# Optimization experiments

Measured on AMD Instinct MI355X. Metric: run time of the kernel, lower is better.

Reference implementation:

```python
import jax, jax.numpy as jnp
import numpy as np

E, TOPK, HID, FFN = 8, 2, 1024, 2048  # experts, top_k, hidden K, intermediate N
B, S = 2, 1024


def setup_inputs() -> dict:
    key = jax.random.key(0)
    ks = jax.random.split(key, 7)
    return {
        "x": jax.random.normal(ks[0], (B, S, HID), jnp.float32),
        "router_weight": jax.random.normal(ks[1], (E, HID), jnp.float32) * 0.02,
        "router_bias": jax.random.normal(ks[2], (E,), jnp.float32) * 0.02,
        "w1": jax.random.normal(ks[3], (E, 2 * FFN, HID), jnp.float32) * 0.02,  # [E,2N,K] gate|up
        "w1_bias": jax.random.normal(ks[4], (E, 2 * FFN), jnp.float32) * 0.02,
        "w2": jax.random.normal(ks[5], (E, HID, FFN), jnp.float32) * 0.02,      # [E,K,N]
        "w2_bias": jax.random.normal(ks[6], (E, HID), jnp.float32) * 0.02,
        "top_k": TOPK,
    }


def reference(x, router_weight, router_bias, w1, w1_bias, w2, w2_bias, top_k):
    Bb, Ss, K = x.shape
    xf = x.reshape(-1, K)                                   # [M,K]
    M = xf.shape[0]
    Ne = w1.shape[0]
    # --- route_tokens: softmax over experts, then top-k (megablocks style) ---
    logits = xf @ router_weight.T + router_bias             # [M,E]
    probs = jax.nn.softmax(logits, axis=-1)
    topk_w, topk_ids = jax.lax.top_k(probs, top_k)          # [M,topk]
    # combine weights: scatter top-k probs into dense [M,E]
    comb = jnp.zeros((M, Ne), xf.dtype).at[jnp.arange(M)[:, None], topk_ids].add(topk_w)
    # --- fused experts (dense combine formulation, same math as grouped GEMM) ---
    gu = jnp.einsum('mk,enk->men', xf, w1) + w1_bias[None]  # [M,E,2N]
    Nf = gu.shape[-1] // 2
    gate, up = gu[..., :Nf], gu[..., Nf:]
    h = jax.nn.silu(gate) * up                              # silu_and_mul (SwiGLU)
    down = jnp.einsum('men,ekn->mek', h, w2) + w2_bias[None]  # [M,E,K]
    out = jnp.einsum('mek,me->mk', down, comb)              # weighted combine
    return out.reshape(Bb, Ss, K), topk_w
```

## Files before the change

kernel.cpp:

```cpp
#include <hip/hip_runtime.h>
#include <hip/hip_bf16.h>
#include <math.h>

#define E_    8
#define HID_  1024
#define FFN_  2048
#define M_    2048
#define NP2_  (E_*M_)

typedef __attribute__((ext_vector_type(8))) short bf16x8;
typedef __attribute__((ext_vector_type(8))) short short8v;
typedef __attribute__((ext_vector_type(4))) float f32x4;
typedef __attribute__((ext_vector_type(4))) int   i32x4;

typedef const __attribute__((address_space(1))) void GVOID;
typedef __attribute__((address_space(3))) void LVOID;

#define VMCNT4 asm volatile("s_waitcnt vmcnt(4)" ::: "memory")
#define VMCNT0 asm volatile("s_waitcnt vmcnt(0)" ::: "memory")

__device__ __forceinline__ short f2bf(float f) {
    union { __hip_bfloat16 b; short s; } u;
    u.b = __float2bfloat16(f);
    return u.s;
}

__device__ __forceinline__ bf16x8 pk8(f32x4 lo, f32x4 hi) {
    unsigned u0, u1, u2, u3;
    asm("v_cvt_pk_bf16_f32 %0, %1, %2" : "=v"(u0) : "v"(lo.x), "v"(lo.y));
    asm("v_cvt_pk_bf16_f32 %0, %1, %2" : "=v"(u1) : "v"(lo.z), "v"(lo.w));
    asm("v_cvt_pk_bf16_f32 %0, %1, %2" : "=v"(u2) : "v"(hi.x), "v"(hi.y));
    asm("v_cvt_pk_bf16_f32 %0, %1, %2" : "=v"(u3) : "v"(hi.z), "v"(hi.w));
    union { i32x4 i; bf16x8 b; } r;
    r.i = (i32x4){(int)u0, (int)u1, (int)u2, (int)u3};
    return r.b;
}

__global__ __launch_bounds__(64) void router_kernel(
    const float* __restrict__ x, const float* __restrict__ rw,
    const float* __restrict__ rb, int* __restrict__ fill,
    int* __restrict__ gtok, float* __restrict__ gwt, int* __restrict__ pos,
    float* __restrict__ topk_out, __hip_bfloat16* __restrict__ xb)
{
    const int m    = blockIdx.x;
    const int lane = threadIdx.x;
    const float4* xm4 = (const float4*)(x + (size_t)m * HID_);

    float4 xv[4];
#pragma unroll
    for (int j = 0; j < 4; ++j) xv[j] = xm4[j*64 + lane];

    short4* xbr = (short4*)(xb + (size_t)m * HID_);
#pragma unroll
    for (int j = 0; j < 4; ++j) {
        short4 o;
        o.x = f2bf(xv[j].x); o.y = f2bf(xv[j].y);
        o.z = f2bf(xv[j].z); o.w = f2bf(xv[j].w);
        xbr[j*64 + lane] = o;
    }

    float lg[E_];
#pragma unroll
    for (int e = 0; e < E_; ++e) {
        const float4* we4 = (const float4*)(rw + e * HID_);
        float s = 0.f;
#pragma unroll
        for (int j = 0; j < 4; ++j) {
            float4 w = we4[j*64 + lane];
            s = fmaf(xv[j].x, w.x, s);
            s = fmaf(xv[j].y, w.y, s);
            s = fmaf(xv[j].z, w.z, s);
            s = fmaf(xv[j].w, w.w, s);
        }
        lg[e] = s;
    }
#pragma unroll
    for (int off = 32; off; off >>= 1)
#pragma unroll
        for (int e = 0; e < E_; ++e) lg[e] += __shfl_xor(lg[e], off);

    if (lane == 0) {
        float l2[E_], p[E_];
        float mx = -1e30f;
#pragma unroll
        for (int e = 0; e < E_; ++e) { l2[e] = lg[e] + rb[e]; mx = fmaxf(mx, l2[e]); }
        float sum = 0.f;
#pragma unroll
        for (int e = 0; e < E_; ++e) { p[e] = expf(l2[e] - mx); sum += p[e]; }
        float inv = 1.f / sum;
#pragma unroll
        for (int e = 0; e < E_; ++e) p[e] *= inv;

        int   i1 = -1, i2 = -1;
        float v1 = -1e30f, v2 = -1e30f;
#pragma unroll
        for (int e = 0; e < E_; ++e) {
            float pe = p[e];
            if (pe > v1)      { v2 = v1; i2 = i1; v1 = pe; i1 = e; }
            else if (pe > v2) { v2 = pe; i2 = e; }
        }
        topk_out[2*m]   = v1;
        topk_out[2*m+1] = v2;
        int p1s = atomicAdd(&fill[i1], 1);
        int s1  = i1*M_ + p1s;
        gtok[s1] = m; gwt[s1] = v1; pos[2*m]   = s1;
        int p2s = atomicAdd(&fill[i2], 1);
        int s2  = i2*M_ + p2s;
        gtok[s2] = m; gwt[s2] = v2; pos[2*m+1] = s2;
    }
}

__global__ __launch_bounds__(256, 3) void gemm1_kernel(
    const __hip_bfloat16* __restrict__ xb, const float* __restrict__ w1,
    const float* __restrict__ w1b, const int* __restrict__ gtok,
    const int* __restrict__ fill, __hip_bfloat16* __restrict__ h,
    const float* __restrict__ w2, __hip_bfloat16* __restrict__ w2bf)
{
    const int e  = blockIdx.z;
    const int ce = fill[e];
    const int t0 = blockIdx.y * 128;

    if (blockIdx.y >= 8) {
        int cid = blockIdx.x + 32*(blockIdx.y - 8) + 256*e;
        const float4* src = (const float4*)w2;
        short8v* dst = (short8v*)w2bf;
        size_t c0 = (size_t)cid * 1024;
#pragma unroll
        for (int u = 0; u < 4; ++u) {
            size_t c = c0 + u*256 + threadIdx.x;
            float4 a = src[2*c];
            float4 b = src[2*c + 1];
            short8v o;
            o[0] = f2bf(a.x); o[1] = f2bf(a.y); o[2] = f2bf(a.z); o[3] = f2bf(a.w);
            o[4] = f2bf(b.x); o[5] = f2bf(b.y); o[6] = f2bf(b.z); o[7] = f2bf(b.w);
            dst[c] = o;
        }
    }

    if (t0 >= ce) return;
    const int n0   = blockIdx.x * 64;
    const int base = e * M_;
    const float* w1e = w1 + (size_t)e * (2*FFN_) * HID_;

    __shared__ __align__(16) __hip_bfloat16 As[2][128*32];
    __shared__ __align__(16) float          Bsf[2][128*32];

    const int tid  = threadIdx.x;
    const int lane = tid & 63;
    const int wid  = tid >> 6;
    const int wm   = wid >> 1;
    const int wn   = wid & 1;
    const int cf   = lane >> 4;

    const __hip_bfloat16* asrc[2];
#pragma unroll
    for (int q = 0; q < 2; ++q) {
        int slot = q*256 + tid;
        int r = slot >> 2, p = slot & 3;
        int c = p ^ ((r >> 1) & 3);
        int rr  = min(t0 + r, ce - 1);
        asrc[q] = xb + (size_t)gtok[base + rr] * HID_ + c*8;
    }
    const float* bsrc[4];
#pragma unroll
    for (int q = 0; q < 4; ++q) {
        int slot = q*256 + tid;
        int r = slot >> 3, p = slot & 7;
        int c = p ^ (r & 7);
        int q2 = r >> 5, s = r & 31;
        int grow = (q2 & 1) ? (FFN_ + n0 + (q2>>1)*32 + s)
                            : (       n0 + (q2>>1)*32 + s);
        bsrc[q] = w1e + (size_t)grow * HID_ + c*4;
    }

    auto STAGE = [&](int b, int k0) {
#pragma unroll
        for (int q = 0; q < 2; ++q)
            __builtin_amdgcn_global_load_lds((GVOID*)(asrc[q] + k0),
                (LVOID*)(&As[b][(q*256 + wid*64)*8]), 16, 0, 0);
#pragma unroll
        for (int q = 0; q < 4; ++q)
            __builtin_amdgcn_global_load_lds((GVOID*)(bsrc[q] + k0),
                (LVOID*)(&Bsf[b][(q*256 + wid*64)*4]), 16, 0, 0);
    };

    f32x4 acc[4][4];
#pragma unroll
    for (int m = 0; m < 4; ++m)
#pragma unroll
        for (int n = 0; n < 4; ++n) acc[m][n] = (f32x4){0.f,0.f,0.f,0.f};

    auto COMPUTE = [&](int cb) {
        bf16x8 af[4], bfr[4];
#pragma unroll
        for (int m = 0; m < 4; ++m) {
            int r = wm*64 + m*16 + (lane & 15);
            int sw = cf ^ ((r >> 1) & 3);
            af[m] = *(bf16x8*)&As[cb][r*32 + sw*8];
        }
#pragma unroll
        for (int n = 0; n < 4; ++n) {
            int r = wn*64 + n*16 + (lane & 15);
            int p0 = (2*cf)     ^ (r & 7);
            int p1 = (2*cf + 1) ^ (r & 7);
            f32x4 lo = *(f32x4*)&Bsf[cb][r*32 + p0*4];
            f32x4 hi = *(f32x4*)&Bsf[cb][r*32 + p1*4];
            bfr[n] = pk8(lo, hi);
        }
        __builtin_amdgcn_s_setprio(1);
#pragma unroll
        for (int m = 0; m < 4; ++m)
#pragma unroll
            for (int n = 0; n < 4; ++n)
                acc[m][n] = __builtin_amdgcn_mfma_f32_16x16x32_bf16(
                    af[m], bfr[n], acc[m][n], 0, 0, 0);
        __builtin_amdgcn_s_setprio(0);
    };

    const int NT = HID_/32;
    STAGE(0, 0);
    __syncthreads();
    for (int t = 0; t < NT; ++t) {
        int cur = t & 1, nxt = cur ^ 1;
        if (t + 1 < NT) STAGE(nxt, (t+1)*32);
        COMPUTE(cur);
        __syncthreads();
    }

    const float* w1be = w1b + e*2*FFN_;
#pragma unroll
    for (int n = 0; n < 2; ++n) {
        int col = n0 + wn*32 + n*16 + (lane & 15);
        float bg = w1be[col];
        float bu = w1be[FFN_ + col];
#pragma unroll
        for (int m = 0; m < 4; ++m) {
            int rb2 = t0 + wm*64 + m*16 + (lane >> 4)*4;
#pragma unroll
            for (int i = 0; i < 4; ++i) {
                int t = rb2 + i;
                if (t < ce) {
                    float g = acc[m][n][i]   + bg;
                    float u = acc[m][n+2][i] + bu;
                    float hv = (g / (1.f + __expf(-g))) * u;
                    h[(size_t)(base + t)*FFN_ + col] = __float2bfloat16(hv);
                }
            }
        }
    }
}

__global__ __launch_bounds__(256, 3) void gemm2_kernel(
    const __hip_bfloat16* __restrict__ h, const __hip_bfloat16* __restrict__ w2bf,
    const float* __restrict__ w2b, const float* __restrict__ gwt,
    const int* __restrict__ fill, float* __restrict__ dpair)
{
    const int e  = blockIdx.z & 7;
    const int ks = blockIdx.z >> 3;
    const int ce = fill[e];
    const int t0 = blockIdx.y * 128;
    if (t0 >= ce) return;
    const int n0    = blockIdx.x * 128;
    const int base  = e * M_;
    const int kbase = ks * (FFN_/2);
    const __hip_bfloat16* w2e = w2bf + (size_t)e * HID_ * FFN_;

    __shared__ __align__(16) __hip_bfloat16 As[3][128*32];
    __shared__ __align__(16) __hip_bfloat16 Bs[3][128*32];

    const int tid  = threadIdx.x;
    const int lane = tid & 63;
    const int wid  = tid >> 6;
    const int wm   = wid >> 1;
    const int wn   = wid & 1;

    const __hip_bfloat16 *asrc[2], *bsrc[2];
#pragma unroll
    for (int q = 0; q < 2; ++q) {
        int slot = q*256 + tid;
        int r = slot >> 2, p = slot & 3;
        int c = p ^ ((r >> 1) & 3);
        int rr = min(t0 + r, ce - 1);
        asrc[q] = h   + (size_t)(base + rr) * FFN_ + kbase + c*8;
        bsrc[q] = w2e + (size_t)(n0 + r)    * FFN_ + kbase + c*8;
    }

    auto STAGE = [&](int b, int k0) {
#pragma unroll
        for (int q = 0; q < 2; ++q)
            __builtin_amdgcn_global_load_lds((GVOID*)(asrc[q] + k0),
                (LVOID*)(&As[b][(q*256 + wid*64)*8]), 16, 0, 0);
#pragma unroll
        for (int q = 0; q < 2; ++q)
            __builtin_amdgcn_global_load_lds((GVOID*)(bsrc[q] + k0),
                (LVOID*)(&Bs[b][(q*256 + wid*64)*8]), 16, 0, 0);
    };

    f32x4 acc[4][4];
#pragma unroll
    for (int m = 0; m < 4; ++m)
#pragma unroll
        for (int n = 0; n < 4; ++n) acc[m][n] = (f32x4){0.f,0.f,0.f,0.f};

    const int cf = lane >> 4;
    auto COMPUTE = [&](int cb) {
        bf16x8 af[4], bfr[4];
#pragma unroll
        for (int m = 0; m < 4; ++m) {
            int r = wm*64 + m*16 + (lane & 15);
            int sw = cf ^ ((r >> 1) & 3);
            af[m] = *(bf16x8*)&As[cb][r*32 + sw*8];
        }
#pragma unroll
        for (int n = 0; n < 4; ++n) {
            int r = wn*64 + n*16 + (lane & 15);
            int sw = cf ^ ((r >> 1) & 3);
            bfr[n] = *(bf16x8*)&Bs[cb][r*32 + sw*8];
        }
        __builtin_amdgcn_s_setprio(1);
#pragma unroll
        for (int m = 0; m < 4; ++m)
#pragma unroll
            for (int n = 0; n < 4; ++n)
                acc[m][n] = __builtin_amdgcn_mfma_f32_16x16x32_bf16(
                    af[m], bfr[n], acc[m][n], 0, 0, 0);
        __builtin_amdgcn_s_setprio(0);
    };

    const int NT = (FFN_/2)/32;
    STAGE(0, 0);
    STAGE(1, 32);
    VMCNT4;
    __builtin_amdgcn_s_barrier();

    int cb = 0;
    for (int t = 0; t < NT-2; ++t) {
        int sb = cb + 2; if (sb >= 3) sb -= 3;
        STAGE(sb, (t+2)*32);
        COMPUTE(cb);
        VMCNT4;
        __builtin_amdgcn_s_barrier();
        if (++cb == 3) cb = 0;
    }
    COMPUTE(cb);
    VMCNT0;
    __builtin_amdgcn_s_barrier();
    if (++cb == 3) cb = 0;
    COMPUTE(cb);

    const float* w2be = w2b + e*HID_;
    float* dpk = dpair + (size_t)ks * NP2_ * HID_;
#pragma unroll
    for (int n = 0; n < 4; ++n) {
        int col = n0 + wn*64 + n*16 + (lane & 15);
        float bias = (ks == 0) ? w2be[col] : 0.f;
#pragma unroll
        for (int m = 0; m < 4; ++m) {
            int rb2 = t0 + wm*64 + m*16 + (lane >> 4)*4;
#pragma unroll
            for (int i = 0; i < 4; ++i) {
                int t = rb2 + i;
                if (t < ce) {
                    int p   = base + t;
                    float w = gwt[p];
                    dpk[(size_t)p*HID_ + col] = w * (acc[m][n][i] + bias);
                }
            }
        }
    }
}

__global__ __launch_bounds__(256) void combine_kernel(
    const float* __restrict__ dpair, const int* __restrict__ pos,
    float* __restrict__ out)
{
    int idx = blockIdx.x * 256 + threadIdx.x;
    int m   = idx >> 8;
    int c4  = (idx & 255) * 4;
    int p0 = pos[2*m], p1 = pos[2*m+1];
    const float* d0 = dpair;
    const float* d1 = dpair + (size_t)NP2_ * HID_;
    float4 a0 = *(const float4*)(d0 + (size_t)p0*HID_ + c4);
    float4 a1 = *(const float4*)(d1 + (size_t)p0*HID_ + c4);
    float4 b0 = *(const float4*)(d0 + (size_t)p1*HID_ + c4);
    float4 b1 = *(const float4*)(d1 + (size_t)p1*HID_ + c4);
    float4 o = make_float4((a0.x+a1.x)+(b0.x+b1.x), (a0.y+a1.y)+(b0.y+b1.y),
                           (a0.z+a1.z)+(b0.z+b1.z), (a0.w+a1.w)+(b0.w+b1.w));
    *(float4*)(out + (size_t)m*HID_ + c4) = o;
}

__global__ __launch_bounds__(256) void gemm1_rs_kernel(
    const __hip_bfloat16* __restrict__ xb, const float* __restrict__ w1,
    const float* __restrict__ w1b, const int* __restrict__ gtok,
    const int* __restrict__ fill, __hip_bfloat16* __restrict__ h)
{
    const int e  = blockIdx.z;
    const int ce = fill[e];
    const int t0 = blockIdx.y * 128;
    if (t0 >= ce) return;
    const int n0   = blockIdx.x * 64;
    const int base = e * M_;
    const float* w1e = w1 + (size_t)e * (2*FFN_) * HID_;

    __shared__ __align__(16) __hip_bfloat16 As[128*64];
    __shared__ __align__(16) __hip_bfloat16 Bs[128*64];

    const int tid  = threadIdx.x;
    const int lane = tid & 63;
    const int wid  = tid >> 6;
    const int wm   = wid >> 1;
    const int wn   = wid & 1;

    const __hip_bfloat16* asrc[4];
#pragma unroll
    for (int q = 0; q < 4; ++q) {
        int slot = q*256 + tid;
        int r = slot >> 3, p = slot & 7;
        int rr  = min(t0 + r, ce - 1);
        int tok = gtok[base + rr];
        int c = p ^ (r & 7);
        asrc[q] = xb + (size_t)tok * HID_ + c*8;
    }

    const int brow = tid >> 1;
    const int hk   = tid & 1;
    const int q2 = brow >> 5, s = brow & 31;
    const int grow = (q2 & 1) ? (FFN_ + n0 + (q2>>1)*32 + s)
                              : (       n0 + (q2>>1)*32 + s);
    const float* bsrc = w1e + (size_t)grow * HID_ + hk*32;

    f32x4 acc[4][4];
#pragma unroll
    for (int m = 0; m < 4; ++m)
#pragma unroll
        for (int n = 0; n < 4; ++n) acc[m][n] = (f32x4){0.f,0.f,0.f,0.f};

    float4 breg[8];
#pragma unroll
    for (int j = 0; j < 8; ++j) breg[j] = *(const float4*)(bsrc + j*4);

    for (int k0 = 0; k0 < HID_; k0 += 64) {
#pragma unroll
        for (int q = 0; q < 4; ++q) {
            __builtin_amdgcn_global_load_lds(
                (GVOID*)(asrc[q] + k0),
                (LVOID*)(&As[(q*256 + wid*64)*8]), 16, 0, 0);
        }
#pragma unroll
        for (int cc = 0; cc < 4; ++cc) {
            union { bf16x8 v; short s8[8]; } u;
            const float* f0 = (const float*)&breg[2*cc];
#pragma unroll
            for (int j = 0; j < 8; ++j) u.s8[j] = f2bf(f0[j]);
            int c = hk*4 + cc, p = c ^ (brow & 7);
            *(bf16x8*)&Bs[brow*64 + p*8] = u.v;
        }
        __syncthreads();

        if (k0 + 64 < HID_) {
#pragma unroll
            for (int j = 0; j < 8; ++j) breg[j] = *(const float4*)(bsrc + (k0+64) + j*4);
        }

        bf16x8 af[4][2], bfr[4][2];
#pragma unroll
        for (int m = 0; m < 4; ++m)
#pragma unroll
            for (int kk = 0; kk < 2; ++kk) {
                int r = wm*64 + m*16 + (lane & 15);
                int c = kk*4 + (lane >> 4), p = c ^ (r & 7);
                af[m][kk] = *(bf16x8*)&As[r*64 + p*8];
            }
#pragma unroll
        for (int n = 0; n < 4; ++n)
#pragma unroll
            for (int kk = 0; kk < 2; ++kk) {
                int r = wn*64 + n*16 + (lane & 15);
                int c = kk*4 + (lane >> 4), p = c ^ (r & 7);
                bfr[n][kk] = *(bf16x8*)&Bs[r*64 + p*8];
            }
#pragma unroll
        for (int kk = 0; kk < 2; ++kk)
#pragma unroll
            for (int m = 0; m < 4; ++m)
#pragma unroll
                for (int n = 0; n < 4; ++n)
                    acc[m][n] = __builtin_amdgcn_mfma_f32_16x16x32_bf16(
                        af[m][kk], bfr[n][kk], acc[m][n], 0, 0, 0);
        __syncthreads();
    }

    const float* w1be = w1b + e*2*FFN_;
#pragma unroll
    for (int n = 0; n < 2; ++n) {
        int col = n0 + wn*32 + n*16 + (lane & 15);
        float bg = w1be[col];
        float bu = w1be[FFN_ + col];
#pragma unroll
        for (int m = 0; m < 4; ++m) {
            int rb2 = t0 + wm*64 + m*16 + (lane >> 4)*4;
#pragma unroll
            for (int i = 0; i < 4; ++i) {
                int t = rb2 + i;
                if (t < ce) {
                    float g = acc[m][n][i]   + bg;
                    float u = acc[m][n+2][i] + bu;
                    float hv = (g / (1.f + __expf(-g))) * u;
                    h[(size_t)(base + t)*FFN_ + col] = __float2bfloat16(hv);
                }
            }
        }
    }
}

__global__ __launch_bounds__(256) void gemm2_rs_kernel(
    const __hip_bfloat16* __restrict__ h, const float* __restrict__ w2,
    const float* __restrict__ w2b, const int* __restrict__ gtok,
    const float* __restrict__ gwt, const int* __restrict__ fill,
    float* __restrict__ out)
{
    const int e  = blockIdx.z;
    const int ce = fill[e];
    const int t0 = blockIdx.y * 128;
    if (t0 >= ce) return;
    const int n0   = blockIdx.x * 128;
    const int base = e * M_;
    const float* w2e = w2 + (size_t)e * HID_ * FFN_;

    __shared__ __align__(16) __hip_bfloat16 As[128*64];
    __shared__ __align__(16) __hip_bfloat16 Bs[128*64];

    const int tid  = threadIdx.x;
    const int lane = tid & 63;
    const int wid  = tid >> 6;
    const int wm   = wid >> 1;
    const int wn   = wid & 1;

    const __hip_bfloat16* asrc[4];
#pragma unroll
    for (int q = 0; q < 4; ++q) {
        int slot = q*256 + tid;
        int r = slot >> 3, p = slot & 7;
        int rr = min(t0 + r, ce - 1);
        int c = p ^ (r & 7);
        asrc[q] = h + (size_t)(base + rr) * FFN_ + c*8;
    }

    const int brow = tid >> 1;
    const int hk   = tid & 1;
    const float* bsrc = w2e + (size_t)(n0 + brow) * FFN_ + hk*32;

    f32x4 acc[4][4];
#pragma unroll
    for (int m = 0; m < 4; ++m)
#pragma unroll
        for (int n = 0; n < 4; ++n) acc[m][n] = (f32x4){0.f,0.f,0.f,0.f};

    float4 breg[8];
#pragma unroll
    for (int j = 0; j < 8; ++j) breg[j] = *(const float4*)(bsrc + j*4);

    for (int k0 = 0; k0 < FFN_; k0 += 64) {
#pragma unroll
        for (int q = 0; q < 4; ++q) {
            __builtin_amdgcn_global_load_lds(
                (GVOID*)(asrc[q] + k0),
                (LVOID*)(&As[(q*256 + wid*64)*8]), 16, 0, 0);
        }
#pragma unroll
        for (int cc = 0; cc < 4; ++cc) {
            union { bf16x8 v; short s8[8]; } u;
            const float* f0 = (const float*)&breg[2*cc];
#pragma unroll
            for (int j = 0; j < 8; ++j) u.s8[j] = f2bf(f0[j]);
            int c = hk*4 + cc, p = c ^ (brow & 7);
            *(bf16x8*)&Bs[brow*64 + p*8] = u.v;
        }
        __syncthreads();

        if (k0 + 64 < FFN_) {
#pragma unroll
            for (int j = 0; j < 8; ++j) breg[j] = *(const float4*)(bsrc + (k0+64) + j*4);
        }

        bf16x8 af[4][2], bfr[4][2];
#pragma unroll
        for (int m = 0; m < 4; ++m)
#pragma unroll
            for (int kk = 0; kk < 2; ++kk) {
                int r = wm*64 + m*16 + (lane & 15);
                int c = kk*4 + (lane >> 4), p = c ^ (r & 7);
                af[m][kk] = *(bf16x8*)&As[r*64 + p*8];
            }
#pragma unroll
        for (int n = 0; n < 4; ++n)
#pragma unroll
            for (int kk = 0; kk < 2; ++kk) {
                int r = wn*64 + n*16 + (lane & 15);
                int c = kk*4 + (lane >> 4), p = c ^ (r & 7);
                bfr[n][kk] = *(bf16x8*)&Bs[r*64 + p*8];
            }
#pragma unroll
        for (int kk = 0; kk < 2; ++kk)
#pragma unroll
            for (int m = 0; m < 4; ++m)
#pragma unroll
                for (int n = 0; n < 4; ++n)
                    acc[m][n] = __builtin_amdgcn_mfma_f32_16x16x32_bf16(
                        af[m][kk], bfr[n][kk], acc[m][n], 0, 0, 0);
        __syncthreads();
    }

    const float* w2be = w2b + e*HID_;
#pragma unroll
    for (int n = 0; n < 4; ++n) {
        int col = n0 + wn*64 + n*16 + (lane & 15);
        float bias = w2be[col];
#pragma unroll
        for (int m = 0; m < 4; ++m) {
            int rb2 = t0 + wm*64 + m*16 + (lane >> 4)*4;
#pragma unroll
            for (int i = 0; i < 4; ++i) {
                int t = rb2 + i;
                if (t < ce) {
                    int p   = base + t;
                    float w = gwt[p];
                    atomicAdd(&out[(size_t)gtok[p]*HID_ + col], w * (acc[m][n][i] + bias));
                }
            }
        }
    }
}

extern "C" void kernel_launch(void* const* d_in, const int* in_sizes, int n_in,
                              void* d_out, int out_size, void* d_ws, size_t ws_size,
                              hipStream_t stream)
{
    const float* x   = (const float*)d_in[0];
    const float* rw  = (const float*)d_in[1];
    const float* rb  = (const float*)d_in[2];
    const float* w1  = (const float*)d_in[3];
    const float* w1b = (const float*)d_in[4];
    const float* w2  = (const float*)d_in[5];
    const float* w2b = (const float*)d_in[6];

    float* out      = (float*)d_out;
    float* topk_out = out + (size_t)M_ * HID_;

    const size_t MB = 1024*1024;
    char*  ws   = (char*)d_ws;
    int*   fill = (int*)  (ws);
    int*   pos  = (int*)  (ws + 128);
    int*   gtok = (int*)  (ws + 65536);
    float* gwt  = (float*)(ws + 131072);
    __hip_bfloat16* xb    = (__hip_bfloat16*)(ws + 1*MB);
    __hip_bfloat16* h     = (__hip_bfloat16*)(ws + 5*MB);
    float*          dpair = (float*)         (ws + 69*MB);
    __hip_bfloat16* w2bf  = (__hip_bfloat16*)(ws + 197*MB);
    const bool tier2 = (ws_size >= 230*MB);

    hipMemsetAsync(fill, 0, E_ * sizeof(int), stream);

    router_kernel<<<M_, 64, 0, stream>>>(x, rw, rb, fill, gtok, gwt, pos,
                                         topk_out, xb);

    if (tier2) {
        dim3 g1(FFN_/64, M_/128, E_);
        gemm1_kernel<<<g1, 256, 0, stream>>>(xb, w1, w1b, gtok, fill, h,
                                             w2, w2bf);

        dim3 g2(HID_/128, M_/128, 2*E_);
        gemm2_kernel<<<g2, 256, 0, stream>>>(h, w2bf, w2b, gwt, fill, dpair);

        combine_kernel<<<(M_*HID_)/(256*4), 256, 0, stream>>>(dpair, pos, out);
    } else {
        hipMemsetAsync(out, 0, (size_t)M_ * HID_ * sizeof(float), stream);

        dim3 g1(FFN_/64, M_/128, E_);
        gemm1_rs_kernel<<<g1, 256, 0, stream>>>(xb, w1, w1b, gtok, fill, h);

        dim3 g2(HID_/128, M_/128, E_);
        gemm2_rs_kernel<<<g2, 256, 0, stream>>>(h, w2, w2b, gtok, gwt, fill, out);
    }
}
```

Baseline: 214.1 us.

## Convert fp32 weights to bf16 in registers before LDS store in both GEMMs

Both expert GEMMs now read fp32 weight tiles into registers, pack them to bf16 and write the bf16 values to LDS. Previously gemm1 staged fp32 into LDS via direct global-to-LDS loads, and a separate pass converted w2 to a bf16 workspace copy. This removes the w2 conversion pass and its extra global traffic, and halves the LDS footprint for B tiles. In exchange, the weight loads become register round trips with the LDS write placed after compute, and gemm2 drops from a 3-stage vmcnt-based pipeline to a 2-stage one synchronised with __syncthreads.

```diff
diff --git a/kernel.cpp b/kernel.cpp
--- a/kernel.cpp
+++ b/kernel.cpp
@@ -9,15 +9,11 @@
 #define NP2_  (E_*M_)
 
 typedef __attribute__((ext_vector_type(8))) short bf16x8;
-typedef __attribute__((ext_vector_type(8))) short short8v;
 typedef __attribute__((ext_vector_type(4))) float f32x4;
 typedef __attribute__((ext_vector_type(4))) int   i32x4;
 
 typedef const __attribute__((address_space(1))) void GVOID;
 typedef __attribute__((address_space(3))) void LVOID;
-
-#define VMCNT4 asm volatile("s_waitcnt vmcnt(4)" ::: "memory")
-#define VMCNT0 asm volatile("s_waitcnt vmcnt(0)" ::: "memory")
 
 __device__ __forceinline__ short f2bf(float f) {
     union { __hip_bfloat16 b; short s; } u;
@@ -25,7 +21,7 @@
     return u.s;
 }
 
-__device__ __forceinline__ bf16x8 pk8(f32x4 lo, f32x4 hi) {
+__device__ __forceinline__ bf16x8 pk8f(float4 lo, float4 hi) {
     unsigned u0, u1, u2, u3;
     asm("v_cvt_pk_bf16_f32 %0, %1, %2" : "=v"(u0) : "v"(lo.x), "v"(lo.y));
     asm("v_cvt_pk_bf16_f32 %0, %1, %2" : "=v"(u1) : "v"(lo.z), "v"(lo.w));
@@ -110,40 +106,22 @@
     }
 }
 
+
 __global__ __launch_bounds__(256, 3) void gemm1_kernel(
     const __hip_bfloat16* __restrict__ xb, const float* __restrict__ w1,
     const float* __restrict__ w1b, const int* __restrict__ gtok,
-    const int* __restrict__ fill, __hip_bfloat16* __restrict__ h,
-    const float* __restrict__ w2, __hip_bfloat16* __restrict__ w2bf)
+    const int* __restrict__ fill, __hip_bfloat16* __restrict__ h)
 {
     const int e  = blockIdx.z;
     const int ce = fill[e];
     const int t0 = blockIdx.y * 128;
-
-    if (blockIdx.y >= 8) {
-        int cid = blockIdx.x + 32*(blockIdx.y - 8) + 256*e;
-        const float4* src = (const float4*)w2;
-        short8v* dst = (short8v*)w2bf;
-        size_t c0 = (size_t)cid * 1024;
-#pragma unroll
-        for (int u = 0; u < 4; ++u) {
-            size_t c = c0 + u*256 + threadIdx.x;
-            float4 a = src[2*c];
-            float4 b = src[2*c + 1];
-            short8v o;
-            o[0] = f2bf(a.x); o[1] = f2bf(a.y); o[2] = f2bf(a.z); o[3] = f2bf(a.w);
-            o[4] = f2bf(b.x); o[5] = f2bf(b.y); o[6] = f2bf(b.z); o[7] = f2bf(b.w);
-            dst[c] = o;
-        }
-    }
-
     if (t0 >= ce) return;
     const int n0   = blockIdx.x * 64;
     const int base = e * M_;
     const float* w1e = w1 + (size_t)e * (2*FFN_) * HID_;
 
     __shared__ __align__(16) __hip_bfloat16 As[2][128*32];
-    __shared__ __align__(16) float          Bsf[2][128*32];
+    __shared__ __align__(16) __hip_bfloat16 Bs[2][128*32];
 
     const int tid  = threadIdx.x;
     const int lane = tid & 63;
@@ -161,27 +139,39 @@
         int rr  = min(t0 + r, ce - 1);
         asrc[q] = xb + (size_t)gtok[base + rr] * HID_ + c*8;
     }
-    const float* bsrc[4];
-#pragma unroll
-    for (int q = 0; q < 4; ++q) {
+    const float* bsrc[2];
+    int bdoff[2];
+#pragma unroll
+    for (int q = 0; q < 2; ++q) {
         int slot = q*256 + tid;
-        int r = slot >> 3, p = slot & 7;
-        int c = p ^ (r & 7);
+        int r = slot >> 2, p = slot & 3;
+        int c = p ^ ((r >> 1) & 3);
         int q2 = r >> 5, s = r & 31;
         int grow = (q2 & 1) ? (FFN_ + n0 + (q2>>1)*32 + s)
                             : (       n0 + (q2>>1)*32 + s);
-        bsrc[q] = w1e + (size_t)grow * HID_ + c*4;
-    }
-
-    auto STAGE = [&](int b, int k0) {
+        bsrc[q]  = w1e + (size_t)grow * HID_ + c*8;
+        bdoff[q] = r*32 + p*8;
+    }
+
+    auto STAGE_A = [&](int b, int k0) {
 #pragma unroll
         for (int q = 0; q < 2; ++q)
             __builtin_amdgcn_global_load_lds((GVOID*)(asrc[q] + k0),
                 (LVOID*)(&As[b][(q*256 + wid*64)*8]), 16, 0, 0);
-#pragma unroll
-        for (int q = 0; q < 4; ++q)
-            __builtin_amdgcn_global_load_lds((GVOID*)(bsrc[q] + k0),
-                (LVOID*)(&Bsf[b][(q*256 + wid*64)*4]), 16, 0, 0);
+    };
+
+    float4 br[2][2];
+    auto BLOAD = [&](int k0) {
+#pragma unroll
+        for (int q = 0; q < 2; ++q) {
+            br[q][0] = *(const float4*)(bsrc[q] + k0);
+            br[q][1] = *(const float4*)(bsrc[q] + k0 + 4);
+        }
+    };
+    auto BWRITE = [&](int b) {
+#pragma unroll
+        for (int q = 0; q < 2; ++q)
+            *(bf16x8*)&Bs[b][bdoff[q]] = pk8f(br[q][0], br[q][1]);
     };
 
     f32x4 acc[4][4];
@@ -201,11 +191,8 @@
 #pragma unroll
         for (int n = 0; n < 4; ++n) {
             int r = wn*64 + n*16 + (lane & 15);
-            int p0 = (2*cf)     ^ (r & 7);
-            int p1 = (2*cf + 1) ^ (r & 7);
-            f32x4 lo = *(f32x4*)&Bsf[cb][r*32 + p0*4];
-            f32x4 hi = *(f32x4*)&Bsf[cb][r*32 + p1*4];
-            bfr[n] = pk8(lo, hi);
+            int sw = cf ^ ((r >> 1) & 3);
+            bfr[n] = *(bf16x8*)&Bs[cb][r*32 + sw*8];
         }
         __builtin_amdgcn_s_setprio(1);
 #pragma unroll
@@ -218,12 +205,15 @@
     };
 
     const int NT = HID_/32;
-    STAGE(0, 0);
+    STAGE_A(0, 0);
+    BLOAD(0);
+    BWRITE(0);
     __syncthreads();
     for (int t = 0; t < NT; ++t) {
         int cur = t & 1, nxt = cur ^ 1;
-        if (t + 1 < NT) STAGE(nxt, (t+1)*32);
+        if (t + 1 < NT) { STAGE_A(nxt, (t+1)*32); BLOAD((t+1)*32); }
         COMPUTE(cur);
+        if (t + 1 < NT) BWRITE(nxt);
         __syncthreads();
     }
 
@@ -251,7 +241,7 @@
 }
 
 __global__ __launch_bounds__(256, 3) void gemm2_kernel(
-    const __hip_bfloat16* __restrict__ h, const __hip_bfloat16* __restrict__ w2bf,
+    const __hip_bfloat16* __restrict__ h, const float* __restrict__ w2,
     const float* __restrict__ w2b, const float* __restrict__ gwt,
     const int* __restrict__ fill, float* __restrict__ dpair)
 {
@@ -263,37 +253,57 @@
     const int n0    = blockIdx.x * 128;
     const int base  = e * M_;
     const int kbase = ks * (FFN_/2);
-    const __hip_bfloat16* w2e = w2bf + (size_t)e * HID_ * FFN_;
-
-    __shared__ __align__(16) __hip_bfloat16 As[3][128*32];
-    __shared__ __align__(16) __hip_bfloat16 Bs[3][128*32];
+    const float* w2e = w2 + (size_t)e * HID_ * FFN_;
+
+    __shared__ __align__(16) __hip_bfloat16 As[2][128*32];
+    __shared__ __align__(16) __hip_bfloat16 Bs[2][128*32];
 
     const int tid  = threadIdx.x;
     const int lane = tid & 63;
     const int wid  = tid >> 6;
     const int wm   = wid >> 1;
     const int wn   = wid & 1;
-
-    const __hip_bfloat16 *asrc[2], *bsrc[2];
+    const int cf   = lane >> 4;
+
+    const __hip_bfloat16* asrc[2];
 #pragma unroll
     for (int q = 0; q < 2; ++q) {
         int slot = q*256 + tid;
         int r = slot >> 2, p = slot & 3;
         int c = p ^ ((r >> 1) & 3);
         int rr = min(t0 + r, ce - 1);
-        asrc[q] = h   + (size_t)(base + rr) * FFN_ + kbase + c*8;
-        bsrc[q] = w2e + (size_t)(n0 + r)    * FFN_ + kbase + c*8;
-    }
-
-    auto STAGE = [&](int b, int k0) {
+        asrc[q] = h + (size_t)(base + rr) * FFN_ + kbase + c*8;
+    }
+    const float* bsrc[2];
+    int bdoff[2];
+#pragma unroll
+    for (int q = 0; q < 2; ++q) {
+        int slot = q*256 + tid;
+        int r = slot >> 2, p = slot & 3;
+        int c = p ^ ((r >> 1) & 3);
+        bsrc[q]  = w2e + (size_t)(n0 + r) * FFN_ + kbase + c*8;
+        bdoff[q] = r*32 + p*8;
+    }
+
+    auto STAGE_A = [&](int b, int k0) {
 #pragma unroll
         for (int q = 0; q < 2; ++q)
             __builtin_amdgcn_global_load_lds((GVOID*)(asrc[q] + k0),
                 (LVOID*)(&As[b][(q*256 + wid*64)*8]), 16, 0, 0);
+    };
+
+    float4 br[2][2];
+    auto BLOAD = [&](int k0) {
+#pragma unroll
+        for (int q = 0; q < 2; ++q) {
+            br[q][0] = *(const float4*)(bsrc[q] + k0);
+            br[q][1] = *(const float4*)(bsrc[q] + k0 + 4);
+        }
+    };
+    auto BWRITE = [&](int b) {
 #pragma unroll
         for (int q = 0; q < 2; ++q)
-            __builtin_amdgcn_global_load_lds((GVOID*)(bsrc[q] + k0),
-                (LVOID*)(&Bs[b][(q*256 + wid*64)*8]), 16, 0, 0);
+            *(bf16x8*)&Bs[b][bdoff[q]] = pk8f(br[q][0], br[q][1]);
     };
 
     f32x4 acc[4][4];
@@ -302,7 +312,6 @@
 #pragma unroll
         for (int n = 0; n < 4; ++n) acc[m][n] = (f32x4){0.f,0.f,0.f,0.f};
 
-    const int cf = lane >> 4;
     auto COMPUTE = [&](int cb) {
         bf16x8 af[4], bfr[4];
 #pragma unroll
@@ -328,25 +337,17 @@
     };
 
     const int NT = (FFN_/2)/32;
-    STAGE(0, 0);
-    STAGE(1, 32);
-    VMCNT4;
-    __builtin_amdgcn_s_barrier();
-
-    int cb = 0;
-    for (int t = 0; t < NT-2; ++t) {
-        int sb = cb + 2; if (sb >= 3) sb -= 3;
-        STAGE(sb, (t+2)*32);
-        COMPUTE(cb);
-        VMCNT4;
-        __builtin_amdgcn_s_barrier();
-        if (++cb == 3) cb = 0;
-    }
-    COMPUTE(cb);
-    VMCNT0;
-    __builtin_amdgcn_s_barrier();
-    if (++cb == 3) cb = 0;
-    COMPUTE(cb);
+    STAGE_A(0, 0);
+    BLOAD(0);
+    BWRITE(0);
+    __syncthreads();
+    for (int t = 0; t < NT; ++t) {
+        int cur = t & 1, nxt = cur ^ 1;
+        if (t + 1 < NT) { STAGE_A(nxt, (t+1)*32); BLOAD((t+1)*32); }
+        COMPUTE(cur);
+        if (t + 1 < NT) BWRITE(nxt);
+        __syncthreads();
+    }
 
     const float* w2be = w2b + e*HID_;
     float* dpk = dpair + (size_t)ks * NP2_ * HID_;
@@ -656,8 +657,7 @@
     __hip_bfloat16* xb    = (__hip_bfloat16*)(ws + 1*MB);
     __hip_bfloat16* h     = (__hip_bfloat16*)(ws + 5*MB);
     float*          dpair = (float*)         (ws + 69*MB);
-    __hip_bfloat16* w2bf  = (__hip_bfloat16*)(ws + 197*MB);
-    const bool tier2 = (ws_size >= 230*MB);
+    const bool tier2 = (ws_size >= 198*MB);
 
     hipMemsetAsync(fill, 0, E_ * sizeof(int), stream);
 
@@ -666,11 +666,10 @@
 
     if (tier2) {
         dim3 g1(FFN_/64, M_/128, E_);
-        gemm1_kernel<<<g1, 256, 0, stream>>>(xb, w1, w1b, gtok, fill, h,
-                                             w2, w2bf);
+        gemm1_kernel<<<g1, 256, 0, stream>>>(xb, w1, w1b, gtok, fill, h);
 
         dim3 g2(HID_/128, M_/128, 2*E_);
-        gemm2_kernel<<<g2, 256, 0, stream>>>(h, w2bf, w2b, gwt, fill, dpair);
+        gemm2_kernel<<<g2, 256, 0, stream>>>(h, w2, w2b, gwt, fill, dpair);
 
         combine_kernel<<<(M_*HID_)/(256*4), 256, 0, stream>>>(dpair, pos, out);
     } else {
```

New measurement: 220.5 us. 3.0% more time.
